# Kernel optimization log

Hardware: AMD Instinct MI355X
Metric: run time of the kernel (lower is better)

Reference implementation:

```python
import jax, jax.numpy as jnp
import numpy as np

D_K = 128
NEG_MAX = float(np.finfo(np.float32).max)  # original uses -finfo(float32).max


def setup_inputs() -> dict:
    key = jax.random.key(0)
    kq, kk, kv, km = jax.random.split(key, 4)
    B, S, D = 16, 2048, D_K
    q = jax.random.normal(kq, (B, S, D), dtype=jnp.float32)
    k = jax.random.normal(kk, (B, S, D), dtype=jnp.float32)
    v = jax.random.normal(kv, (B, S, D), dtype=jnp.float32)
    mask = jax.random.randint(km, (B, S, S), 0, 2).astype(jnp.bool_)
    return {"q": q, "k": k, "v": v, "mask": mask}


def reference(q, k, v, mask):
    # scores: [B, S, S] = q @ k^T / sqrt(d_k)
    scale = 1.0 / np.sqrt(D_K).astype(np.float32)
    scores = jnp.einsum('bqd,bkd->bqk', q, k) * scale
    scores = jnp.where(mask, -NEG_MAX, scores)  # masked_fill with -float32 max
    attn = jax.nn.softmax(scores, axis=2)
    return jnp.einsum('bqk,bkd->bqd', attn, v)
```

## Files before the change

kernel.cpp:

```cpp
#include <hip/hip_runtime.h>

#define NTHREADS 256

typedef __attribute__((ext_vector_type(8))) short bf16x8;
typedef __attribute__((ext_vector_type(4))) float f32x4;
typedef __attribute__((ext_vector_type(2))) unsigned uint2v;
typedef __attribute__((ext_vector_type(4))) unsigned uint4v;

constexpr int kB = 16, kS = 2048, kD = 128;
constexpr int QBLK = 64, KBLK = 64, NROUNDS = kS / KBLK;
constexpr int MSTRIDE = 68;
constexpr float kNegMax = -3.402823466e38f;
constexpr float kMClamp = -1e30f;

__device__ __forceinline__ unsigned cvt_pk(float lo, float hi) {
    unsigned r;
    asm("v_cvt_pk_bf16_f32 %0, %1, %2" : "=v"(r) : "v"(lo), "v"(hi));
    return r;
}

#define SWZ(bytecol, row) ((bytecol) ^ (((row) & 7) << 4))
#define SWZV(bytecol, row) ((bytecol) ^ (((((row) & 7) ^ (((row) >> 2) & 7)) & 7) << 4))
#define SWZP(bytecol, row) ((bytecol) ^ (((row) & 7) << 4))

__global__ __launch_bounds__(NTHREADS, 2)
void attn_fwd(const float* __restrict__ q, const float* __restrict__ k,
              const float* __restrict__ v, const int* __restrict__ mask,
              float* __restrict__ out)
{
    __shared__ __align__(16) char smem[45312];
    char* K_lds  = smem;
    char* VT_lds = smem + 16384;
    char* P_lds  = smem + 32768;
    unsigned char* M_lds = (unsigned char*)(smem + 40960);

    const int tid = threadIdx.x, lane = tid & 63, w = tid >> 6;
    const int l15 = lane & 15, lg = lane >> 4;

    const int bid = (int)blockIdx.x;
    const int swz = (bid & 7) * 64 + (bid >> 3);
    const int b = swz >> 5;
    const int qbase = (swz & 31) * QBLK;

    const float scale = 0.08838834764831845f;
    bf16x8 qf[4];
    {
        const float* qp = q + ((size_t)(b*kS + qbase + w*16 + l15)) * kD;
        #pragma unroll
        for (int kk = 0; kk < 4; ++kk) {
            float4 a = *(const float4*)(qp + kk*32 + lg*8);
            float4 c = *(const float4*)(qp + kk*32 + lg*8 + 4);
            uint4v pk = { cvt_pk(a.x*scale, a.y*scale), cvt_pk(a.z*scale, a.w*scale),
                          cvt_pk(c.x*scale, c.y*scale), cvt_pk(c.z*scale, c.w*scale) };
            qf[kk] = __builtin_bit_cast(bf16x8, pk);
        }
    }

    f32x4 acc[8];
    #pragma unroll
    for (int d = 0; d < 8; ++d) acc[d] = f32x4{0.f,0.f,0.f,0.f};
    float m_r = kMClamp, l_r = 0.f;

    const float* kbat = k + (size_t)b * kS * kD;
    const float* vbat = v + (size_t)b * kS * kD;
    const int*   mbat = mask + ((size_t)b * kS + qbase) * kS;

    char* Pw = P_lds + w * 2048;

    float4 kreg[4][2];
    float4 vreg[2][4];
    int4   mreg[4];

    auto LOAD = [&](int kt0) {
        #pragma unroll
        for (int c = 0; c < 4; ++c) {
            int chunk = c * 256 + tid;
            int row = chunk >> 4, col8 = chunk & 15;
            const float4* ptr = (const float4*)(kbat + (size_t)(kt0 + row)*kD + col8*8);
            kreg[c][0] = ptr[0];
            kreg[c][1] = ptr[1];
        }
        #pragma unroll
        for (int it = 0; it < 2; ++it) {
            int blk = it * 256 + tid;
            int kg = blk >> 5, dg = blk & 31;
            #pragma unroll
            for (int r = 0; r < 4; ++r)
                vreg[it][r] = *(const float4*)(vbat + (size_t)(kt0 + kg*4 + r)*kD + dg*4);
        }
        #pragma unroll
        for (int c = 0; c < 4; ++c) {
            int idx = c * 256 + tid;
            int mrow = idx >> 4, mc4 = idx & 15;
            mreg[c] = *(const int4*)(mbat + (size_t)mrow*kS + kt0 + mc4*4);
        }
    };

    auto STORE = [&]() {
        #pragma unroll
        for (int c = 0; c < 4; ++c) {
            int chunk = c * 256 + tid;
            int row = chunk >> 4, col8 = chunk & 15;
            uint4v pk = { cvt_pk(kreg[c][0].x, kreg[c][0].y), cvt_pk(kreg[c][0].z, kreg[c][0].w),
                          cvt_pk(kreg[c][1].x, kreg[c][1].y), cvt_pk(kreg[c][1].z, kreg[c][1].w) };
            *(uint4v*)(K_lds + row*256 + SWZ(col8*16, row)) = pk;
        }
        #pragma unroll
        for (int it = 0; it < 2; ++it) {
            int blk = it * 256 + tid;
            int kg = blk >> 5, dg = blk & 31;
            #pragma unroll
            for (int jj = 0; jj < 4; ++jj) {
                int row = dg * 4 + jj;
                uint2v pk = { cvt_pk((&vreg[it][0].x)[jj], (&vreg[it][1].x)[jj]),
                              cvt_pk((&vreg[it][2].x)[jj], (&vreg[it][3].x)[jj]) };
                *(uint2v*)(VT_lds + row*128 + SWZV(kg*8, row)) = pk;
            }
        }
        #pragma unroll
        for (int c = 0; c < 4; ++c) {
            int idx = c * 256 + tid;
            int mrow = idx >> 4, mc4 = idx & 15;
            unsigned pk = (unsigned)(mreg[c].x != 0)
                        | ((unsigned)(mreg[c].y != 0) << 8)
                        | ((unsigned)(mreg[c].z != 0) << 16)
                        | ((unsigned)(mreg[c].w != 0) << 24);
            *(unsigned*)(M_lds + mrow*MSTRIDE + mc4*4) = pk;
        }
    };

    LOAD(0);

    for (int t = 0; t < NROUNDS; ++t) {
        __syncthreads();
        STORE();
        __syncthreads();
        if (t + 1 < NROUNDS) LOAD((t + 1) * KBLK);

        f32x4 z[4];
        #pragma unroll
        for (int kt = 0; kt < 4; ++kt) {
            f32x4 zz = f32x4{0.f,0.f,0.f,0.f};
            int krow = kt*16 + l15;
            #pragma unroll
            for (int kk = 0; kk < 4; ++kk) {
                bf16x8 kf = *(const bf16x8*)(K_lds + krow*256 + SWZ(kk*64 + lg*16, krow));
                zz = __builtin_amdgcn_mfma_f32_16x16x32_bf16(kf, qf[kk], zz, 0, 0, 0);
            }
            z[kt] = zz;
        }

        const int mrowb = (w*16 + l15) * MSTRIDE;
        float mx = kNegMax;
        #pragma unroll
        for (int kt = 0; kt < 4; ++kt) {
            unsigned nib = *(const unsigned*)(M_lds + mrowb + kt*16 + lg*4);
            #pragma unroll
            for (int i = 0; i < 4; ++i) {
                float sv = ((nib >> (8*i)) & 0xFFu) ? kNegMax : z[kt][i];
                z[kt][i] = sv;
                mx = fmaxf(mx, sv);
            }
        }
        mx = fmaxf(mx, __shfl_xor(mx, 16));
        mx = fmaxf(mx, __shfl_xor(mx, 32));
        float mnew = fmaxf(m_r, mx);
        float corr = __expf(m_r - mnew);
        float rs = 0.f;
        #pragma unroll
        for (int kt = 0; kt < 4; ++kt) {
            float p0 = __expf(z[kt][0] - mnew);
            float p1 = __expf(z[kt][1] - mnew);
            float p2 = __expf(z[kt][2] - mnew);
            float p3 = __expf(z[kt][3] - mnew);
            rs += (p0 + p1) + (p2 + p3);
            uint2v pk = { cvt_pk(p0, p1), cvt_pk(p2, p3) };
            *(uint2v*)(Pw + l15*128 + SWZP(kt*32 + lg*8, l15)) = pk;
        }
        rs += __shfl_xor(rs, 16);
        rs += __shfl_xor(rs, 32);
        m_r = mnew;
        l_r = l_r * corr + rs;
        #pragma unroll
        for (int d = 0; d < 8; ++d) acc[d] *= corr;

        #pragma unroll
        for (int ks = 0; ks < 2; ++ks) {
            bf16x8 pf = *(const bf16x8*)(Pw + l15*128 + SWZP(ks*64 + lg*16, l15));
            #pragma unroll
            for (int dblk = 0; dblk < 8; ++dblk) {
                int vrow = dblk*16 + l15;
                bf16x8 vf = *(const bf16x8*)(VT_lds + vrow*128 + SWZV(ks*64 + lg*16, vrow));
                acc[dblk] = __builtin_amdgcn_mfma_f32_16x16x32_bf16(vf, pf, acc[dblk], 0, 0, 0);
            }
        }
    }

    float inv = 1.0f / l_r;
    float* op = out + ((size_t)(b*kS + qbase + w*16 + l15)) * kD;
    #pragma unroll
    for (int dblk = 0; dblk < 8; ++dblk) {
        float4 r;
        r.x = acc[dblk][0] * inv;
        r.y = acc[dblk][1] * inv;
        r.z = acc[dblk][2] * inv;
        r.w = acc[dblk][3] * inv;
        *(float4*)(op + dblk*16 + lg*4) = r;
    }
}

extern "C" void kernel_launch(void* const* d_in, const int* in_sizes, int n_in,
                              void* d_out, int out_size, void* d_ws, size_t ws_size,
                              hipStream_t stream) {
    const float* q = (const float*)d_in[0];
    const float* k = (const float*)d_in[1];
    const float* v = (const float*)d_in[2];
    const int* mask = (const int*)d_in[3];
    float* out = (float*)d_out;
    dim3 grid(kB * (kS / QBLK));
    dim3 block(NTHREADS);
    attn_fwd<<<grid, block, 0, stream>>>(q, k, v, mask, out);
}
```

Before: 115.7 us.

## Split key range in two per query block and merge partials in second kernel

Each query block's key sequence is split into two halves processed by separate workgroups. Each half writes unnormalized accumulators plus running max and sum to a workspace. A merge kernel then combines them with log-sum-exp rescaling. The aim is more workgroups and parallelism, at the cost of extra workspace traffic and a second launch. It falls back to the single-pass kernel if the workspace is too small.

```diff
diff --git a/kernel.cpp b/kernel.cpp
--- a/kernel.cpp
+++ b/kernel.cpp
@@ -8,7 +8,7 @@
 typedef __attribute__((ext_vector_type(4))) unsigned uint4v;
 
 constexpr int kB = 16, kS = 2048, kD = 128;
-constexpr int QBLK = 64, KBLK = 64, NROUNDS = kS / KBLK;
+constexpr int QBLK = 64, KBLK = 64;
 constexpr int MSTRIDE = 68;
 constexpr float kNegMax = -3.402823466e38f;
 constexpr float kMClamp = -1e30f;
@@ -23,10 +23,11 @@
 #define SWZV(bytecol, row) ((bytecol) ^ (((((row) & 7) ^ (((row) >> 2) & 7)) & 7) << 4))
 #define SWZP(bytecol, row) ((bytecol) ^ (((row) & 7) << 4))
 
+template<int SPLIT>
 __global__ __launch_bounds__(NTHREADS, 2)
 void attn_fwd(const float* __restrict__ q, const float* __restrict__ k,
               const float* __restrict__ v, const int* __restrict__ mask,
-              float* __restrict__ out)
+              float* __restrict__ out, float* __restrict__ ws)
 {
     __shared__ __align__(16) char smem[45312];
     char* K_lds  = smem;
@@ -38,9 +39,18 @@
     const int l15 = lane & 15, lg = lane >> 4;
 
     const int bid = (int)blockIdx.x;
-    const int swz = (bid & 7) * 64 + (bid >> 3);
-    const int b = swz >> 5;
-    const int qbase = (swz & 31) * QBLK;
+    int b, qbase, kbase;
+    if (SPLIT == 1) {
+        int swz = (bid & 7) * 64 + (bid >> 3);
+        b = swz >> 5; qbase = (swz & 31) * QBLK; kbase = 0;
+    } else {
+        int swz = (bid & 7) * 128 + (bid >> 3);
+        b = swz >> 6;
+        int rem = swz & 63;
+        qbase = (rem >> 1) * QBLK;
+        kbase = (rem & 1) * (kS / 2);
+    }
+    const int nrounds = (SPLIT == 1) ? (kS / KBLK) : (kS / KBLK / 2);
 
     const float scale = 0.08838834764831845f;
     bf16x8 qf[4];
@@ -129,13 +139,13 @@
         }
     };
 
-    LOAD(0);
-
-    for (int t = 0; t < NROUNDS; ++t) {
+    LOAD(kbase);
+
+    for (int t = 0; t < nrounds; ++t) {
         __syncthreads();
         STORE();
         __syncthreads();
-        if (t + 1 < NROUNDS) LOAD((t + 1) * KBLK);
+        if (t + 1 < nrounds) LOAD(kbase + (t + 1) * KBLK);
 
         f32x4 z[4];
         #pragma unroll
@@ -196,17 +206,57 @@
         }
     }
 
-    float inv = 1.0f / l_r;
-    float* op = out + ((size_t)(b*kS + qbase + w*16 + l15)) * kD;
-    #pragma unroll
-    for (int dblk = 0; dblk < 8; ++dblk) {
-        float4 r;
-        r.x = acc[dblk][0] * inv;
-        r.y = acc[dblk][1] * inv;
-        r.z = acc[dblk][2] * inv;
-        r.w = acc[dblk][3] * inv;
-        *(float4*)(op + dblk*16 + lg*4) = r;
-    }
+    if (SPLIT == 1) {
+        float inv = 1.0f / l_r;
+        float* op = out + ((size_t)(b*kS + qbase + w*16 + l15)) * kD;
+        #pragma unroll
+        for (int dblk = 0; dblk < 8; ++dblk) {
+            float4 r;
+            r.x = acc[dblk][0] * inv;
+            r.y = acc[dblk][1] * inv;
+            r.z = acc[dblk][2] * inv;
+            r.w = acc[dblk][3] * inv;
+            *(float4*)(op + dblk*16 + lg*4) = r;
+        }
+    } else {
+        const int half = (kbase != 0);
+        const size_t row = (size_t)half * (kB*kS) + (size_t)b*kS + qbase + w*16 + l15;
+        float* op = ws + row * kD;
+        #pragma unroll
+        for (int dblk = 0; dblk < 8; ++dblk) {
+            float4 r;
+            r.x = acc[dblk][0]; r.y = acc[dblk][1];
+            r.z = acc[dblk][2]; r.w = acc[dblk][3];
+            *(float4*)(op + dblk*16 + lg*4) = r;
+        }
+        if (lg == 0) {
+            float* ml = ws + (size_t)2*kB*kS*kD;
+            ml[row*2 + 0] = m_r;
+            ml[row*2 + 1] = l_r;
+        }
+    }
+}
+
+__global__ __launch_bounds__(NTHREADS)
+void attn_merge(const float* __restrict__ ws, float* __restrict__ out)
+{
+    const float* ml = ws + (size_t)2*kB*kS*kD;
+    const int tid = threadIdx.x;
+    const size_t r = (size_t)blockIdx.x * 8 + (tid >> 5);
+    const int c = (tid & 31) * 4;
+    float m0 = ml[r*2 + 0],               l0 = ml[r*2 + 1];
+    float m1 = ml[((size_t)kB*kS + r)*2], l1 = ml[((size_t)kB*kS + r)*2 + 1];
+    float mS = fmaxf(m0, m1);
+    float e0 = __expf(m0 - mS), e1 = __expf(m1 - mS);
+    float inv = 1.0f / (l0*e0 + l1*e1);
+    float4 o0 = *(const float4*)(ws + r*kD + c);
+    float4 o1 = *(const float4*)(ws + (size_t)kB*kS*kD + r*kD + c);
+    float4 rr;
+    rr.x = (o0.x*e0 + o1.x*e1) * inv;
+    rr.y = (o0.y*e0 + o1.y*e1) * inv;
+    rr.z = (o0.z*e0 + o1.z*e1) * inv;
+    rr.w = (o0.w*e0 + o1.w*e1) * inv;
+    *(float4*)(out + r*kD + c) = rr;
 }
 
 extern "C" void kernel_launch(void* const* d_in, const int* in_sizes, int n_in,
@@ -217,7 +267,13 @@
     const float* v = (const float*)d_in[2];
     const int* mask = (const int*)d_in[3];
     float* out = (float*)d_out;
-    dim3 grid(kB * (kS / QBLK));
-    dim3 block(NTHREADS);
-    attn_fwd<<<grid, block, 0, stream>>>(q, k, v, mask, out);
-}
+    const size_t wsNeeded = (size_t)2*kB*kS*kD*4 + (size_t)2*kB*kS*2*4;
+    if (ws_size >= wsNeeded) {
+        attn_fwd<2><<<dim3(kB * (kS/QBLK) * 2), dim3(NTHREADS), 0, stream>>>(
+            q, k, v, mask, out, (float*)d_ws);
+        attn_merge<<<dim3(kB*kS/8), dim3(NTHREADS), 0, stream>>>((const float*)d_ws, out);
+    } else {
+        attn_fwd<1><<<dim3(kB * (kS/QBLK)), dim3(NTHREADS), 0, stream>>>(
+            q, k, v, mask, out, nullptr);
+    }
+}
```

Result: slower. 120.6 us (+4.2%).
